# Kernel optimization log

Measured on AMD Instinct MI355X. Metric: run time of the kernel, lower is better.

Reference implementation:

```python
import jax, jax.numpy as jnp
import numpy as np

N_HEADS = 16
HEAD_SIZE = 64
D_EMBD = 1024
BLOCK_SIZE = 1024
B, T = 4, 1024


def setup_inputs() -> dict:
    key = jax.random.key(0)
    ks = jax.random.split(key, 6)
    s = 0.02
    x = jax.random.normal(ks[0], (B, T, D_EMBD), dtype=jnp.float32)
    # per-head bias-free Q/K/V projections, stacked: [H, C, Hs]
    Wq = jax.random.normal(ks[1], (N_HEADS, D_EMBD, HEAD_SIZE), dtype=jnp.float32) * s
    Wk = jax.random.normal(ks[2], (N_HEADS, D_EMBD, HEAD_SIZE), dtype=jnp.float32) * s
    Wv = jax.random.normal(ks[3], (N_HEADS, D_EMBD, HEAD_SIZE), dtype=jnp.float32) * s
    # output projection W_o: Linear(d_embd, d_embd) with bias
    Wo = jax.random.normal(ks[4], (D_EMBD, D_EMBD), dtype=jnp.float32) * s
    bo = jax.random.normal(ks[5], (D_EMBD,), dtype=jnp.float32) * s
    return {"x": x, "Wq": Wq, "Wk": Wk, "Wv": Wv, "Wo": Wo, "bo": bo}


def reference(x, Wq, Wk, Wv, Wo, bo):
    # Batched equivalent of the per-head loop: q,k,v: [B, H, T, Hs]
    q = jnp.einsum('btc,hcs->bhts', x, Wq)
    k = jnp.einsum('btc,hcs->bhts', x, Wk)
    v = jnp.einsum('btc,hcs->bhts', x, Wv)
    scale = 1.0 / jnp.sqrt(jnp.asarray(HEAD_SIZE, dtype=x.dtype))
    scores = jnp.einsum('bhts,bhus->bhtu', q, k) * scale  # [B,H,T,T]
    causal = jnp.tril(jnp.ones((T, T), dtype=bool))
    scores = jnp.where(causal[None, None, :, :], scores, jnp.asarray(-jnp.inf, dtype=x.dtype))
    wei = jax.nn.softmax(scores, axis=-1)  # dropout p=0.0 -> identity
    out = jnp.einsum('bhtu,bhus->bhts', wei, v)  # [B,H,T,Hs]
    out = out.transpose(0, 2, 1, 3).reshape(B, T, D_EMBD)  # concat heads
    return out @ Wo.T + bo  # final Linear; dropout p=0.0 -> identity
```

## Files before the change

kernel.cpp:

```cpp
#include <hip/hip_runtime.h>
#include <hip/hip_bf16.h>
#include <math.h>

#define NH 16
#define HS 64
#define DE 1024
#define TT 1024
#define BBATCH 4
#define MTOK 4096

typedef __bf16 v8bf __attribute__((ext_vector_type(8)));
typedef __bf16 v4bf __attribute__((ext_vector_type(4)));
typedef float  v4f  __attribute__((ext_vector_type(4)));

__device__ __forceinline__ void gl_lds16(const __bf16* g, __bf16* l) {
    __builtin_amdgcn_global_load_lds(
        (const __attribute__((address_space(1))) unsigned int*)g,
        (__attribute__((address_space(3))) unsigned int*)l, 16, 0, 0);
}

__global__ __launch_bounds__(256) void prep_all_kernel(
    const float* __restrict__ x,  __bf16* __restrict__ xb,
    const float* __restrict__ Wo, __bf16* __restrict__ Wob,
    const float* __restrict__ Wq, const float* __restrict__ Wk,
    const float* __restrict__ Wv, __bf16* __restrict__ Wt)
{
    const int bid = blockIdx.x;
    const int t = threadIdx.x;
    if (bid < 5120) {
        int i = bid * 256 + t;
        const float* in; __bf16* out;
        if (i < 1048576) { in = x;  out = xb; }
        else             { in = Wo; out = Wob; i -= 1048576; }
        float4 v = ((const float4*)in)[i];
        v4bf o;
        o[0] = (__bf16)v.x; o[1] = (__bf16)v.y; o[2] = (__bf16)v.z; o[3] = (__bf16)v.w;
        *(v4bf*)&out[(size_t)i * 4] = o;
        return;
    }
    const int bid2 = bid - 5120;
    const int c0 = (bid2 & 15) * 64, h = (bid2 >> 4) & 15, m = bid2 >> 8;
    const float* W = (m == 0) ? Wq : (m == 1) ? Wk : Wv;
    __shared__ float tile[64][65];
    #pragma unroll
    for (int pp = 0; pp < 16; ++pp) {
        int cl = pp * 4 + (t >> 6);
        int s  = t & 63;
        tile[cl][s] = W[((size_t)h * DE + c0 + cl) * HS + s];
    }
    __syncthreads();
    #pragma unroll
    for (int pp = 0; pp < 16; ++pp) {
        int s  = pp * 4 + (t >> 6);
        int cl = t & 63;
        Wt[((size_t)(m * DE + h * HS + s)) * DE + c0 + cl] = (__bf16)tile[cl][s];
    }
}

__device__ __forceinline__ void gemm_stage(
    const __bf16* __restrict__ Ab, const __bf16* __restrict__ Bb,
    __bf16* As, __bf16* Bs, int K, int k0, int w, int l)
{
    #pragma unroll
    for (int i = 0; i < 4; ++i) {
        int p   = i * 256 + w * 64 + l;
        int row = p >> 3;
        int lc  = (p & 7) ^ (row & 7);
        gl_lds16(Ab + (size_t)row * K + k0 + lc * 8, As + p * 8);
        gl_lds16(Bb + (size_t)row * K + k0 + lc * 8, Bs + p * 8);
    }
}

__global__ __launch_bounds__(256) void gemm_bt_kernel(
    const __bf16* __restrict__ A, const __bf16* __restrict__ Bt,
    int K,
    __bf16* __restrict__ qk_out, __bf16* __restrict__ vt_out)
{
    __shared__ __align__(16) __bf16 As[128 * 64];
    __shared__ __align__(16) __bf16 Bs[128 * 64];
    const int tid = threadIdx.x;
    const int w = tid >> 6, l = tid & 63;
    const int wm = w >> 1, wn = w & 1;
    const int lhi = l >> 4, llo = l & 15;
    const int sw0 = ((lhi ^ (llo & 7)) << 3);
    const int sw1 = sw0 ^ 32;

    const int lin = blockIdx.x;
    const int xcd = lin & 7, j = lin >> 3;
    const int bm = xcd * 4 + (j & 3);
    const int bn = j >> 2;

    v4f acc[4][4];
    #pragma unroll
    for (int i = 0; i < 4; ++i)
        #pragma unroll
        for (int jj = 0; jj < 4; ++jj)
            #pragma unroll
            for (int r = 0; r < 4; ++r) acc[i][jj][r] = 0.f;

    const __bf16* Ab = A  + (size_t)bm * 128 * K;
    const __bf16* Bb = Bt + (size_t)bn * 128 * K;

    const int niter = K >> 6;
    for (int it = 0; it < niter; ++it) {
        if (it) __syncthreads();
        gemm_stage(Ab, Bb, As, Bs, K, it * 64, w, l);
        __syncthreads();
        #pragma unroll
        for (int kk = 0; kk < 64; kk += 32) {
            const int sw = kk ? sw1 : sw0;
            v8bf a[4], b[4];
            #pragma unroll
            for (int i = 0; i < 4; ++i)
                a[i] = *(const v8bf*)&As[(wm * 64 + i * 16 + llo) * 64 + sw];
            #pragma unroll
            for (int jj = 0; jj < 4; ++jj)
                b[jj] = *(const v8bf*)&Bs[(wn * 64 + jj * 16 + llo) * 64 + sw];
            #pragma unroll
            for (int i = 0; i < 4; ++i)
                #pragma unroll
                for (int jj = 0; jj < 4; ++jj)
                    acc[i][jj] = __builtin_amdgcn_mfma_f32_16x16x32_bf16(a[i], b[jj], acc[i][jj], 0, 0, 0);
        }
    }

    const int row0 = bm * 128 + wm * 64;
    const int col0 = bn * 128 + wn * 64;

    if (col0 < 2048) {
        #pragma unroll
        for (int i = 0; i < 4; ++i) {
            int rbase = row0 + i * 16 + lhi * 4;
            #pragma unroll
            for (int jj = 0; jj < 4; ++jj) {
                int c = col0 + jj * 16 + llo;
                #pragma unroll
                for (int r = 0; r < 4; ++r)
                    qk_out[(size_t)(rbase + r) * 2048 + c] = (__bf16)acc[i][jj][r];
            }
        }
    } else {
        #pragma unroll
        for (int i = 0; i < 4; ++i) {
            int rbase = row0 + i * 16 + lhi * 4;
            int bidx = rbase >> 10, t0 = rbase & 1023;
            #pragma unroll
            for (int jj = 0; jj < 4; ++jj) {
                int c = col0 + jj * 16 + llo - 2048;
                v4bf pk;
                #pragma unroll
                for (int r = 0; r < 4; ++r) pk[r] = (__bf16)acc[i][jj][r];
                *(v4bf*)&vt_out[((size_t)(bidx * NH + (c >> 6)) * HS + (c & 63)) * TT + t0] = pk;
            }
        }
    }
}

__global__ __launch_bounds__(256) void gemm_bt64_kernel(
    const __bf16* __restrict__ A, const __bf16* __restrict__ Bt, int K,
    float* __restrict__ f_out, const float* __restrict__ bias)
{
    __shared__ __align__(16) __bf16 As[2][64 * 64];
    __shared__ __align__(16) __bf16 Bs[2][128 * 64];
    const int tid = threadIdx.x;
    const int w = tid >> 6, l = tid & 63;
    const int wm = w & 1, wn = w >> 1;
    const int lhi = l >> 4, llo = l & 15;
    const int sw0 = ((lhi ^ (llo & 7)) << 3);
    const int sw1 = sw0 ^ 32;

    const int lin = blockIdx.x;
    const int xcd = lin & 7, j = lin >> 3;
    const int bm = xcd * 8 + (j & 7);
    const int bn = j >> 3;

    v4f acc[2][4];
    #pragma unroll
    for (int i = 0; i < 2; ++i)
        #pragma unroll
        for (int jj = 0; jj < 4; ++jj)
            #pragma unroll
            for (int r = 0; r < 4; ++r) acc[i][jj][r] = 0.f;

    const __bf16* Ab = A  + (size_t)bm * 64 * K;
    const __bf16* Bb = Bt + (size_t)bn * 128 * K;

    const int niter = K >> 6;
    {
        #pragma unroll
        for (int i = 0; i < 2; ++i) {
            int p = i * 256 + tid, row = p >> 3, lc = (p & 7) ^ (row & 7);
            gl_lds16(Ab + (size_t)row * K + lc * 8, As[0] + p * 8);
        }
        #pragma unroll
        for (int i = 0; i < 4; ++i) {
            int p = i * 256 + tid, row = p >> 3, lc = (p & 7) ^ (row & 7);
            gl_lds16(Bb + (size_t)row * K + lc * 8, Bs[0] + p * 8);
        }
    }

    for (int it = 0; it < niter; ++it) {
        const int buf = it & 1;
        __syncthreads();
        if (it + 1 < niter) {
            const int k0 = (it + 1) * 64;
            #pragma unroll
            for (int i = 0; i < 2; ++i) {
                int p = i * 256 + tid, row = p >> 3, lc = (p & 7) ^ (row & 7);
                gl_lds16(Ab + (size_t)row * K + k0 + lc * 8, As[buf ^ 1] + p * 8);
            }
            #pragma unroll
            for (int i = 0; i < 4; ++i) {
                int p = i * 256 + tid, row = p >> 3, lc = (p & 7) ^ (row & 7);
                gl_lds16(Bb + (size_t)row * K + k0 + lc * 8, Bs[buf ^ 1] + p * 8);
            }
        }
        #pragma unroll
        for (int kk = 0; kk < 64; kk += 32) {
            const int sw = kk ? sw1 : sw0;
            v8bf a[2], b[4];
            #pragma unroll
            for (int i = 0; i < 2; ++i)
                a[i] = *(const v8bf*)&As[buf][(wm * 32 + i * 16 + llo) * 64 + sw];
            #pragma unroll
            for (int jj = 0; jj < 4; ++jj)
                b[jj] = *(const v8bf*)&Bs[buf][(wn * 64 + jj * 16 + llo) * 64 + sw];
            #pragma unroll
            for (int i = 0; i < 2; ++i)
                #pragma unroll
                for (int jj = 0; jj < 4; ++jj)
                    acc[i][jj] = __builtin_amdgcn_mfma_f32_16x16x32_bf16(a[i], b[jj], acc[i][jj], 0, 0, 0);
        }
    }

    const int row0 = bm * 64 + wm * 32;
    const int col0 = bn * 128 + wn * 64;
    #pragma unroll
    for (int jj = 0; jj < 4; ++jj) {
        int c = col0 + jj * 16 + llo;
        float bv = bias[c];
        #pragma unroll
        for (int i = 0; i < 2; ++i) {
            int rbase = row0 + i * 16 + lhi * 4;
            #pragma unroll
            for (int r = 0; r < 4; ++r)
                f_out[(size_t)(rbase + r) * DE + c] = acc[i][jj][r] + bv;
        }
    }
}

__device__ __forceinline__ v4f bf_mfma(v8bf a, v8bf b, v4f c) {
    return __builtin_amdgcn_mfma_f32_16x16x32_bf16(a, b, c, 0, 0, 0);
}

__device__ __forceinline__ void stage_kv(
    const __bf16* __restrict__ kb, const __bf16* __restrict__ vb,
    __bf16* Ksb, __bf16* Vsb, int k0, int tid)
{
    #pragma unroll
    for (int i = 0; i < 2; ++i) {
        int p   = i * 256 + tid;
        int row = p >> 3;
        int lc  = (p & 7) ^ (row & 7);
        gl_lds16(kb + (size_t)(k0 + row) * 2048 + lc * 8, Ksb + p * 8);
        gl_lds16(vb + (size_t)row * TT + k0 + lc * 8,     Vsb + p * 8);
    }
}

template<bool DIAG>
__device__ __forceinline__ void attn_compute(
    const __bf16* __restrict__ Ksb, const __bf16* __restrict__ Vsb,
    __bf16* __restrict__ PsW, int k0, int r0, int lhi, int llo, int sw0, int sw1,
    v8bf aq0, v8bf aq1, v4f (&o)[4], float (&l_part)[4])
{
    v4f sacc[4];
    #pragma unroll
    for (int n = 0; n < 4; ++n)
        #pragma unroll
        for (int r = 0; r < 4; ++r) sacc[n][r] = 0.f;
    #pragma unroll
    for (int n = 0; n < 4; ++n) {
        v8bf bk0 = *(const v8bf*)&Ksb[(n * 16 + llo) * 64 + sw0];
        v8bf bk1 = *(const v8bf*)&Ksb[(n * 16 + llo) * 64 + sw1];
        sacc[n] = bf_mfma(aq0, bk0, sacc[n]);
        sacc[n] = bf_mfma(aq1, bk1, sacc[n]);
    }

    float prob[4][4];
    #pragma unroll
    for (int n = 0; n < 4; ++n) {
        int colg = k0 + n * 16 + llo;
        #pragma unroll
        for (int r = 0; r < 4; ++r) {
            float s2 = sacc[n][r] * 0.18033688f;
            if (DIAG) { int rowg = r0 + lhi * 4 + r; if (colg > rowg) s2 = -1e30f; }
            float p = exp2f(s2);
            prob[n][r] = p;
            l_part[r] += p;
        }
    }

    #pragma unroll
    for (int r = 0; r < 4; ++r)
        #pragma unroll
        for (int n = 0; n < 4; ++n)
            PsW[(lhi * 4 + r) * 72 + n * 16 + llo] = (__bf16)prob[n][r];

    #pragma unroll
    for (int kk = 0; kk < 64; kk += 32) {
        v8bf ap = *(const v8bf*)&PsW[llo * 72 + kk + lhi * 8];
        const int sw = kk ? sw1 : sw0;
        #pragma unroll
        for (int n = 0; n < 4; ++n) {
            v8bf bv = *(const v8bf*)&Vsb[(n * 16 + llo) * 64 + sw];
            o[n] = bf_mfma(ap, bv, o[n]);
        }
    }
}

__global__ __launch_bounds__(256) void attn_kernel(
    const __bf16* __restrict__ qk, const __bf16* __restrict__ vt,
    __bf16* __restrict__ att)
{
    __shared__ __align__(16) __bf16 Ks[2][64 * 64];
    __shared__ __align__(16) __bf16 Vs[2][64 * 64];
    __shared__ __align__(16) __bf16 Ps[4][16 * 72];

    const int tid = threadIdx.x;
    const int w = tid >> 6, l = tid & 63;
    const int lhi = l >> 4, llo = l & 15;
    const int sw0 = ((lhi ^ (llo & 7)) << 3);
    const int sw1 = sw0 ^ 32;
    const int bh = blockIdx.x & 63;
    const int qt = 15 - (blockIdx.x >> 6);
    const int b = bh >> 4, h = bh & 15;

    const __bf16* qbase = qk + (size_t)b * TT * 2048 + h * HS;
    const __bf16* kbase = qk + (size_t)b * TT * 2048 + 1024 + h * HS;
    const __bf16* vbase = vt + (size_t)bh * HS * TT;
    __bf16* PsW = &Ps[w][0];

    const int r0 = qt * 64 + w * 16;

    stage_kv(kbase, vbase, Ks[0], Vs[0], 0, tid);

    v8bf aq0 = *(const v8bf*)&qbase[(size_t)(r0 + llo) * 2048 + lhi * 8];
    v8bf aq1 = *(const v8bf*)&qbase[(size_t)(r0 + llo) * 2048 + 32 + lhi * 8];

    float l_part[4] = {0.f, 0.f, 0.f, 0.f};
    v4f o[4];
    #pragma unroll
    for (int n = 0; n < 4; ++n)
        #pragma unroll
        for (int r = 0; r < 4; ++r) o[n][r] = 0.f;

    for (int kt = 0; kt < qt; ++kt) {
        const int buf = kt & 1;
        __syncthreads();
        stage_kv(kbase, vbase, Ks[buf ^ 1], Vs[buf ^ 1], (kt + 1) * 64, tid);
        attn_compute<false>(Ks[buf], Vs[buf], PsW, kt * 64, r0, lhi, llo, sw0, sw1, aq0, aq1, o, l_part);
    }
    __syncthreads();
    attn_compute<true>(Ks[qt & 1], Vs[qt & 1], PsW, qt * 64, r0, lhi, llo, sw0, sw1, aq0, aq1, o, l_part);

    #pragma unroll
    for (int r = 0; r < 4; ++r) {
        float s = l_part[r];
        #pragma unroll
        for (int msk = 1; msk < 16; msk <<= 1) s += __shfl_xor(s, msk, 64);
        float inv = 1.f / s;
        int rowg = b * TT + r0 + lhi * 4 + r;
        #pragma unroll
        for (int n = 0; n < 4; ++n)
            att[(size_t)rowg * DE + h * HS + n * 16 + llo] = (__bf16)(o[n][r] * inv);
    }
}

extern "C" void kernel_launch(void* const* d_in, const int* in_sizes, int n_in,
                              void* d_out, int out_size, void* d_ws, size_t ws_size,
                              hipStream_t stream)
{
    const float* x  = (const float*)d_in[0];
    const float* Wq = (const float*)d_in[1];
    const float* Wk = (const float*)d_in[2];
    const float* Wv = (const float*)d_in[3];
    const float* Wo = (const float*)d_in[4];
    const float* bo = (const float*)d_in[5];
    float* out = (float*)d_out;

    char* ws = (char*)d_ws;
    __bf16* xb  = (__bf16*)(ws);
    __bf16* Wt  = (__bf16*)(ws + 8388608);
    __bf16* Wob = (__bf16*)(ws + 14680064);
    __bf16* qk  = (__bf16*)(ws + 16777216);
    __bf16* vt  = (__bf16*)(ws + 33554432);
    __bf16* att = (__bf16*)(ws + 41943040);

    prep_all_kernel<<<5888, 256, 0, stream>>>(x, xb, Wo, Wob, Wq, Wk, Wv, Wt);
    gemm_bt_kernel<<<768, 256, 0, stream>>>(xb, Wt, 1024, qk, vt);
    attn_kernel<<<1024, 256, 0, stream>>>(qk, vt, att);
    gemm_bt64_kernel<<<512, 256, 0, stream>>>(att, Wob, 1024, out, bo);
}
```

Before: 155.4 us.

## Load K/V tiles directly from global memory in attention, dropping LDS staging

Removes the double-buffered LDS staging of K and V tiles and the per-iteration block barriers. Each wave now reads its K and V MFMA operands straight from global memory into registers and raises wave priority around the MFMA bursts. This aims to cut barrier and LDS traffic overhead. The cost is that all four waves redundantly fetch the same K/V data through the caches, and loads are no longer prefetched a tile ahead.

```diff
diff --git a/kernel.cpp b/kernel.cpp
--- a/kernel.cpp
+++ b/kernel.cpp
@@ -253,24 +253,10 @@
     return __builtin_amdgcn_mfma_f32_16x16x32_bf16(a, b, c, 0, 0, 0);
 }
 
-__device__ __forceinline__ void stage_kv(
+template<bool DIAG>
+__device__ __forceinline__ void attn_compute_g(
     const __bf16* __restrict__ kb, const __bf16* __restrict__ vb,
-    __bf16* Ksb, __bf16* Vsb, int k0, int tid)
-{
-    #pragma unroll
-    for (int i = 0; i < 2; ++i) {
-        int p   = i * 256 + tid;
-        int row = p >> 3;
-        int lc  = (p & 7) ^ (row & 7);
-        gl_lds16(kb + (size_t)(k0 + row) * 2048 + lc * 8, Ksb + p * 8);
-        gl_lds16(vb + (size_t)row * TT + k0 + lc * 8,     Vsb + p * 8);
-    }
-}
-
-template<bool DIAG>
-__device__ __forceinline__ void attn_compute(
-    const __bf16* __restrict__ Ksb, const __bf16* __restrict__ Vsb,
-    __bf16* __restrict__ PsW, int k0, int r0, int lhi, int llo, int sw0, int sw1,
+    __bf16* __restrict__ PsW, int k0, int r0, int lhi, int llo,
     v8bf aq0, v8bf aq1, v4f (&o)[4], float (&l_part)[4])
 {
     v4f sacc[4];
@@ -278,13 +264,20 @@
     for (int n = 0; n < 4; ++n)
         #pragma unroll
         for (int r = 0; r < 4; ++r) sacc[n][r] = 0.f;
+
+    v8bf bk0[4], bk1[4];
     #pragma unroll
     for (int n = 0; n < 4; ++n) {
-        v8bf bk0 = *(const v8bf*)&Ksb[(n * 16 + llo) * 64 + sw0];
-        v8bf bk1 = *(const v8bf*)&Ksb[(n * 16 + llo) * 64 + sw1];
-        sacc[n] = bf_mfma(aq0, bk0, sacc[n]);
-        sacc[n] = bf_mfma(aq1, bk1, sacc[n]);
-    }
+        bk0[n] = *(const v8bf*)&kb[(size_t)(k0 + n * 16 + llo) * 2048 + lhi * 8];
+        bk1[n] = *(const v8bf*)&kb[(size_t)(k0 + n * 16 + llo) * 2048 + 32 + lhi * 8];
+    }
+    __builtin_amdgcn_s_setprio(1);
+    #pragma unroll
+    for (int n = 0; n < 4; ++n) {
+        sacc[n] = bf_mfma(aq0, bk0[n], sacc[n]);
+        sacc[n] = bf_mfma(aq1, bk1[n], sacc[n]);
+    }
+    __builtin_amdgcn_s_setprio(0);
 
     float prob[4][4];
     #pragma unroll
@@ -309,12 +302,15 @@
     #pragma unroll
     for (int kk = 0; kk < 64; kk += 32) {
         v8bf ap = *(const v8bf*)&PsW[llo * 72 + kk + lhi * 8];
-        const int sw = kk ? sw1 : sw0;
-        #pragma unroll
-        for (int n = 0; n < 4; ++n) {
-            v8bf bv = *(const v8bf*)&Vsb[(n * 16 + llo) * 64 + sw];
-            o[n] = bf_mfma(ap, bv, o[n]);
-        }
+        v8bf bv[4];
+        #pragma unroll
+        for (int n = 0; n < 4; ++n)
+            bv[n] = *(const v8bf*)&vb[(size_t)(n * 16 + llo) * TT + k0 + kk + lhi * 8];
+        __builtin_amdgcn_s_setprio(1);
+        #pragma unroll
+        for (int n = 0; n < 4; ++n)
+            o[n] = bf_mfma(ap, bv[n], o[n]);
+        __builtin_amdgcn_s_setprio(0);
     }
 }
 
@@ -322,15 +318,11 @@
     const __bf16* __restrict__ qk, const __bf16* __restrict__ vt,
     __bf16* __restrict__ att)
 {
-    __shared__ __align__(16) __bf16 Ks[2][64 * 64];
-    __shared__ __align__(16) __bf16 Vs[2][64 * 64];
     __shared__ __align__(16) __bf16 Ps[4][16 * 72];
 
     const int tid = threadIdx.x;
     const int w = tid >> 6, l = tid & 63;
     const int lhi = l >> 4, llo = l & 15;
-    const int sw0 = ((lhi ^ (llo & 7)) << 3);
-    const int sw1 = sw0 ^ 32;
     const int bh = blockIdx.x & 63;
     const int qt = 15 - (blockIdx.x >> 6);
     const int b = bh >> 4, h = bh & 15;
@@ -342,8 +334,6 @@
 
     const int r0 = qt * 64 + w * 16;
 
-    stage_kv(kbase, vbase, Ks[0], Vs[0], 0, tid);
-
     v8bf aq0 = *(const v8bf*)&qbase[(size_t)(r0 + llo) * 2048 + lhi * 8];
     v8bf aq1 = *(const v8bf*)&qbase[(size_t)(r0 + llo) * 2048 + 32 + lhi * 8];
 
@@ -354,14 +344,9 @@
         #pragma unroll
         for (int r = 0; r < 4; ++r) o[n][r] = 0.f;
 
-    for (int kt = 0; kt < qt; ++kt) {
-        const int buf = kt & 1;
-        __syncthreads();
-        stage_kv(kbase, vbase, Ks[buf ^ 1], Vs[buf ^ 1], (kt + 1) * 64, tid);
-        attn_compute<false>(Ks[buf], Vs[buf], PsW, kt * 64, r0, lhi, llo, sw0, sw1, aq0, aq1, o, l_part);
-    }
-    __syncthreads();
-    attn_compute<true>(Ks[qt & 1], Vs[qt & 1], PsW, qt * 64, r0, lhi, llo, sw0, sw1, aq0, aq1, o, l_part);
+    for (int kt = 0; kt < qt; ++kt)
+        attn_compute_g<false>(kbase, vbase, PsW, kt * 64, r0, lhi, llo, aq0, aq1, o, l_part);
+    attn_compute_g<true>(kbase, vbase, PsW, qt * 64, r0, lhi, llo, aq0, aq1, o, l_part);
 
     #pragma unroll
     for (int r = 0; r < 4; ++r) {
```

Measured after the change: 197.7 us. +27.2%, slower.

## Enlarge attention query tile to 128 rows so each K/V tile is reused twice

Applied to the files above, without the earlier changes.

Each block now handles 128 query rows, with each wave owning two 16-row groups, where before it handled 64. Every staged K/V tile is therefore reused across twice as many rows, and K/V fragments are loaded from LDS once per tile and shared by both groups. This halves the global K/V traffic and the number of blocks (1024 to 512). Causal skipping is done per group. The trade-offs are more registers, a larger LDS buffer for P, and a coarser and less even work split across the causal triangle with fewer blocks.

```diff
diff --git a/kernel.cpp b/kernel.cpp
--- a/kernel.cpp
+++ b/kernel.cpp
@@ -267,53 +267,64 @@
     }
 }
 
-template<bool DIAG>
-__device__ __forceinline__ void attn_compute(
+__device__ __forceinline__ void attn_tile(
     const __bf16* __restrict__ Ksb, const __bf16* __restrict__ Vsb,
-    __bf16* __restrict__ PsW, int k0, int r0, int lhi, int llo, int sw0, int sw1,
-    v8bf aq0, v8bf aq1, v4f (&o)[4], float (&l_part)[4])
-{
-    v4f sacc[4];
-    #pragma unroll
-    for (int n = 0; n < 4; ++n)
-        #pragma unroll
-        for (int r = 0; r < 4; ++r) sacc[n][r] = 0.f;
+    __bf16* __restrict__ PsW,
+    int k0, int rw0, int lhi, int llo, int sw0, int sw1,
+    const v8bf (&aq)[2][2], v4f (&o)[2][4], float (&l_part)[2][4])
+{
+    if (k0 >= rw0 + 32) return;
+
+    v8bf bk0[4], bk1[4];
     #pragma unroll
     for (int n = 0; n < 4; ++n) {
-        v8bf bk0 = *(const v8bf*)&Ksb[(n * 16 + llo) * 64 + sw0];
-        v8bf bk1 = *(const v8bf*)&Ksb[(n * 16 + llo) * 64 + sw1];
-        sacc[n] = bf_mfma(aq0, bk0, sacc[n]);
-        sacc[n] = bf_mfma(aq1, bk1, sacc[n]);
-    }
-
-    float prob[4][4];
-    #pragma unroll
-    for (int n = 0; n < 4; ++n) {
-        int colg = k0 + n * 16 + llo;
-        #pragma unroll
-        for (int r = 0; r < 4; ++r) {
-            float s2 = sacc[n][r] * 0.18033688f;
-            if (DIAG) { int rowg = r0 + lhi * 4 + r; if (colg > rowg) s2 = -1e30f; }
-            float p = exp2f(s2);
-            prob[n][r] = p;
-            l_part[r] += p;
-        }
-    }
-
-    #pragma unroll
-    for (int r = 0; r < 4; ++r)
+        bk0[n] = *(const v8bf*)&Ksb[(n * 16 + llo) * 64 + sw0];
+        bk1[n] = *(const v8bf*)&Ksb[(n * 16 + llo) * 64 + sw1];
+    }
+
+    #pragma unroll
+    for (int g = 0; g < 2; ++g) {
+        const int rg0 = rw0 + g * 16;
+        if (k0 >= rg0 + 16) continue;
+        const bool mask = (k0 + 64 > rg0);
+        v4f sacc[4];
         #pragma unroll
         for (int n = 0; n < 4; ++n)
-            PsW[(lhi * 4 + r) * 72 + n * 16 + llo] = (__bf16)prob[n][r];
+            #pragma unroll
+            for (int r = 0; r < 4; ++r) sacc[n][r] = 0.f;
+        #pragma unroll
+        for (int n = 0; n < 4; ++n) {
+            sacc[n] = bf_mfma(aq[g][0], bk0[n], sacc[n]);
+            sacc[n] = bf_mfma(aq[g][1], bk1[n], sacc[n]);
+        }
+        #pragma unroll
+        for (int n = 0; n < 4; ++n) {
+            int colg = k0 + n * 16 + llo;
+            #pragma unroll
+            for (int r = 0; r < 4; ++r) {
+                float s2 = sacc[n][r] * 0.18033688f;
+                if (mask) { int rowg = rg0 + lhi * 4 + r; if (colg > rowg) s2 = -1e30f; }
+                float p = exp2f(s2);
+                l_part[g][r] += p;
+                PsW[g * 1152 + (lhi * 4 + r) * 72 + n * 16 + llo] = (__bf16)p;
+            }
+        }
+    }
 
     #pragma unroll
     for (int kk = 0; kk < 64; kk += 32) {
-        v8bf ap = *(const v8bf*)&PsW[llo * 72 + kk + lhi * 8];
         const int sw = kk ? sw1 : sw0;
-        #pragma unroll
-        for (int n = 0; n < 4; ++n) {
-            v8bf bv = *(const v8bf*)&Vsb[(n * 16 + llo) * 64 + sw];
-            o[n] = bf_mfma(ap, bv, o[n]);
+        v8bf bv[4];
+        #pragma unroll
+        for (int n = 0; n < 4; ++n)
+            bv[n] = *(const v8bf*)&Vsb[(n * 16 + llo) * 64 + sw];
+        #pragma unroll
+        for (int g = 0; g < 2; ++g) {
+            if (k0 >= rw0 + g * 16 + 16) continue;
+            v8bf ap = *(const v8bf*)&PsW[g * 1152 + llo * 72 + kk + lhi * 8];
+            #pragma unroll
+            for (int n = 0; n < 4; ++n)
+                o[g][n] = bf_mfma(ap, bv[n], o[g][n]);
         }
     }
 }
@@ -324,7 +335,7 @@
 {
     __shared__ __align__(16) __bf16 Ks[2][64 * 64];
     __shared__ __align__(16) __bf16 Vs[2][64 * 64];
-    __shared__ __align__(16) __bf16 Ps[4][16 * 72];
+    __shared__ __align__(16) __bf16 Ps[4][2 * 1152];
 
     const int tid = threadIdx.x;
     const int w = tid >> 6, l = tid & 63;
@@ -332,7 +343,7 @@
     const int sw0 = ((lhi ^ (llo & 7)) << 3);
     const int sw1 = sw0 ^ 32;
     const int bh = blockIdx.x & 63;
-    const int qt = 15 - (blockIdx.x >> 6);
+    const int qs = 7 - (blockIdx.x >> 6);
     const int b = bh >> 4, h = bh & 15;
 
     const __bf16* qbase = qk + (size_t)b * TT * 2048 + h * HS;
@@ -340,40 +351,51 @@
     const __bf16* vbase = vt + (size_t)bh * HS * TT;
     __bf16* PsW = &Ps[w][0];
 
-    const int r0 = qt * 64 + w * 16;
+    const int rw0 = qs * 128 + w * 32;
+    const int nt = 2 * qs + 2;
+
+    v8bf aq[2][2];
+    #pragma unroll
+    for (int g = 0; g < 2; ++g) {
+        aq[g][0] = *(const v8bf*)&qbase[(size_t)(rw0 + g * 16 + llo) * 2048 + lhi * 8];
+        aq[g][1] = *(const v8bf*)&qbase[(size_t)(rw0 + g * 16 + llo) * 2048 + 32 + lhi * 8];
+    }
+
+    float l_part[2][4];
+    v4f o[2][4];
+    #pragma unroll
+    for (int g = 0; g < 2; ++g)
+        #pragma unroll
+        for (int n = 0; n < 4; ++n) {
+            l_part[g][n] = 0.f;
+            #pragma unroll
+            for (int r = 0; r < 4; ++r) o[g][n][r] = 0.f;
+        }
 
     stage_kv(kbase, vbase, Ks[0], Vs[0], 0, tid);
 
-    v8bf aq0 = *(const v8bf*)&qbase[(size_t)(r0 + llo) * 2048 + lhi * 8];
-    v8bf aq1 = *(const v8bf*)&qbase[(size_t)(r0 + llo) * 2048 + 32 + lhi * 8];
-
-    float l_part[4] = {0.f, 0.f, 0.f, 0.f};
-    v4f o[4];
-    #pragma unroll
-    for (int n = 0; n < 4; ++n)
-        #pragma unroll
-        for (int r = 0; r < 4; ++r) o[n][r] = 0.f;
-
-    for (int kt = 0; kt < qt; ++kt) {
+    for (int kt = 0; kt < nt - 1; ++kt) {
         const int buf = kt & 1;
         __syncthreads();
         stage_kv(kbase, vbase, Ks[buf ^ 1], Vs[buf ^ 1], (kt + 1) * 64, tid);
-        attn_compute<false>(Ks[buf], Vs[buf], PsW, kt * 64, r0, lhi, llo, sw0, sw1, aq0, aq1, o, l_part);
+        attn_tile(Ks[buf], Vs[buf], PsW, kt * 64, rw0, lhi, llo, sw0, sw1, aq, o, l_part);
     }
     __syncthreads();
-    attn_compute<true>(Ks[qt & 1], Vs[qt & 1], PsW, qt * 64, r0, lhi, llo, sw0, sw1, aq0, aq1, o, l_part);
-
-    #pragma unroll
-    for (int r = 0; r < 4; ++r) {
-        float s = l_part[r];
-        #pragma unroll
-        for (int msk = 1; msk < 16; msk <<= 1) s += __shfl_xor(s, msk, 64);
-        float inv = 1.f / s;
-        int rowg = b * TT + r0 + lhi * 4 + r;
-        #pragma unroll
-        for (int n = 0; n < 4; ++n)
-            att[(size_t)rowg * DE + h * HS + n * 16 + llo] = (__bf16)(o[n][r] * inv);
-    }
+    attn_tile(Ks[(nt - 1) & 1], Vs[(nt - 1) & 1], PsW, (nt - 1) * 64, rw0, lhi, llo, sw0, sw1, aq, o, l_part);
+
+    #pragma unroll
+    for (int g = 0; g < 2; ++g)
+        #pragma unroll
+        for (int r = 0; r < 4; ++r) {
+            float s = l_part[g][r];
+            #pragma unroll
+            for (int msk = 1; msk < 16; msk <<= 1) s += __shfl_xor(s, msk, 64);
+            float inv = 1.f / s;
+            int rowg = b * TT + rw0 + g * 16 + lhi * 4 + r;
+            #pragma unroll
+            for (int n = 0; n < 4; ++n)
+                att[(size_t)rowg * DE + h * HS + n * 16 + llo] = (__bf16)(o[g][n][r] * inv);
+        }
 }
 
 extern "C" void kernel_launch(void* const* d_in, const int* in_sizes, int n_in,
@@ -398,6 +420,6 @@
 
     prep_all_kernel<<<5888, 256, 0, stream>>>(x, xb, Wo, Wob, Wq, Wk, Wv, Wt);
     gemm_bt_kernel<<<768, 256, 0, stream>>>(xb, Wt, 1024, qk, vt);
-    attn_kernel<<<1024, 256, 0, stream>>>(qk, vt, att);
+    attn_kernel<<<512, 256, 0, stream>>>(qk, vt, att);
     gemm_bt64_kernel<<<512, 256, 0, stream>>>(att, Wob, 1024, out, bo);
 }
```

After: 169.4 us. 1.09x slower.
